# Optimization experiments

Measured on AMD Instinct MI355X. Metric: run time of the kernel, lower is better.

## Reference

```python
import jax, jax.numpy as jnp
import numpy as np

TEMPERATURE = 0.07


def setup_inputs() -> dict:
    key = jax.random.key(0)
    k1, k2, k3 = jax.random.split(key, 3)
    b, num_proposals, num_phrases, f = 128, 100, 16, 512
    img_features = jax.random.normal(k1, (b, num_proposals, f), dtype=jnp.float32)
    text_features = jax.random.normal(k2, (b, num_phrases, f), dtype=jnp.float32)
    labels = jax.random.randint(k3, (b, b), 0, 2, dtype=jnp.int64)
    return {"img_features": img_features, "text_features": text_features, "labels": labels}


def reference(img_features, text_features, labels):
    # att_matrix[b,d,t,i] = <text[b,t,:], img[d,i,:]>
    att_matrix = jnp.einsum('btf,dif->bdti', text_features, img_features)
    argmax_box = att_matrix.max(axis=3)        # [b, d, t]  max over proposals
    score_matrix = argmax_box.mean(axis=2)     # [b, d]     mean over phrases
    score_exp = jnp.exp(score_matrix / TEMPERATURE)
    return score_exp
```

## Files before the change

kernel.cpp:

```cpp
#include <hip/hip_runtime.h>
#include <hip/hip_bf16.h>
#include <stdint.h>


typedef __attribute__((ext_vector_type(4))) int    v4i;
typedef __attribute__((ext_vector_type(8))) int    v8i;
typedef __attribute__((ext_vector_type(4))) float  f32x4;

constexpr int Bb = 128;
constexpr int P  = 100;
constexpr int T  = 16;
constexpr int F  = 512;
constexpr float TEMP = 0.07f;

constexpr int BM   = 128;
constexpr int NCG  = 7;
constexpr int GSZ  = 16 * 16 * 32;
constexpr int NXCD = 8;

__global__ __launch_bounds__(256)
void cvt2_kernel(const float* __restrict__ img, const float* __restrict__ txt,
                 uint8_t* __restrict__ imgb, uint8_t* __restrict__ txtb) {
  __shared__ __align__(16) uint8_t lds[16 * 528];
  const int g  = blockIdx.x;
  const int t  = threadIdx.x;
  const int lr = t >> 4;
  const int c  = t & 15;

  const float* src;
  uint8_t* dst;
  if (g < Bb * NCG) {
    const int d  = g / NCG;
    const int cg = g - d * NCG;
    const int row  = cg * 16 + lr;
    const int prow = row < P ? row : (P - 1);
    src = img + ((size_t)d * P + prow) * F + c * 32;
    dst = imgb + (size_t)g * GSZ;
  } else {
    const int rg = g - Bb * NCG;
    src = txt + ((size_t)rg * 16 + lr) * F + c * 32;
    dst = txtb + (size_t)rg * GSZ;
  }

  int wd[8];
  #pragma unroll
  for (int j = 0; j < 4; j++) {
    float4 v0 = *(const float4*)(src + j * 8);
    float4 v1 = *(const float4*)(src + j * 8 + 4);
    int lo = __builtin_amdgcn_cvt_pk_fp8_f32(v0.x, v0.y, 0, false);
    lo     = __builtin_amdgcn_cvt_pk_fp8_f32(v0.z, v0.w, lo, true);
    int hi = __builtin_amdgcn_cvt_pk_fp8_f32(v1.x, v1.y, 0, false);
    hi     = __builtin_amdgcn_cvt_pk_fp8_f32(v1.z, v1.w, hi, true);
    wd[j * 2] = lo; wd[j * 2 + 1] = hi;
  }
  uint8_t* lp = &lds[lr * 528 + c * 32];
  *(v4i*)lp        = v4i{wd[0], wd[1], wd[2], wd[3]};
  *(v4i*)(lp + 16) = v4i{wd[4], wd[5], wd[6], wd[7]};
  __syncthreads();

  const uint8_t* rp = &lds[(t & 15) * 528 + (t >> 4) * 32];
  v4i lo = *(const v4i*)rp;
  v4i hi = *(const v4i*)(rp + 16);
  *(v4i*)(dst + t * 32)      = lo;
  *(v4i*)(dst + t * 32 + 16) = hi;
}

template<bool FUSED>
__global__ __launch_bounds__(256)
void score_kernel(const void* __restrict__ imgp, const void* __restrict__ txtp,
                  float* __restrict__ out) {
  __shared__ float red[BM][2];

  const int L    = blockIdx.x;
  const int xcd  = L & (NXCD - 1);
  const int slot = L >> 3;
  const int d    = xcd * 16 + (slot >> 4);
  const int b0   = (slot & 15) * (BM / T);

  const int tid  = threadIdx.x;
  const int lane = tid & 63;
  const int w    = tid >> 6;
  const int q    = lane >> 4;
  const int n    = lane & 15;
  const int mh   = w & 1;
  const int nh   = w >> 1;
  const int NCT  = 4 - nh;

  f32x4 acc[4][4] = {};

  if constexpr (!FUSED) {
    const uint8_t* gt = (const uint8_t*)txtp;
    const uint8_t* gi = (const uint8_t*)imgp;
    int agrp[4], bgrp[4];
    #pragma unroll
    for (int rt = 0; rt < 4; rt++) agrp[rt] = b0 + mh * 4 + rt;
    #pragma unroll
    for (int ct = 0; ct < 4; ct++) bgrp[ct] = d * NCG + nh * 4 + ct;

    #pragma unroll
    for (int k4 = 0; k4 < 4; k4++) {
      const int kc  = k4 * 4 + q;
      const int off = kc * 512 + n * 32;
      v8i a[4];
      #pragma unroll
      for (int rt = 0; rt < 4; rt++) {
        const uint8_t* p = gt + (size_t)agrp[rt] * GSZ + off;
        v4i lo = *(const v4i*)p;
        v4i hi = *(const v4i*)(p + 16);
        a[rt] = __builtin_shufflevector(lo, hi, 0, 1, 2, 3, 4, 5, 6, 7);
      }
      #pragma unroll
      for (int ct = 0; ct < 4; ct++) {
        if (ct < NCT) {
          const uint8_t* p = gi + (size_t)bgrp[ct] * GSZ + off;
          v4i lo = *(const v4i*)p;
          v4i hi = *(const v4i*)(p + 16);
          v8i b = __builtin_shufflevector(lo, hi, 0, 1, 2, 3, 4, 5, 6, 7);
          __builtin_amdgcn_s_setprio(1);
          #pragma unroll
          for (int rt = 0; rt < 4; rt++)
            acc[rt][ct] = __builtin_amdgcn_mfma_scale_f32_16x16x128_f8f6f4(
                a[rt], b, acc[rt][ct], 0, 0, 0, 127, 0, 127);
          __builtin_amdgcn_s_setprio(0);
        }
      }
    }
  } else {
    auto frag32 = [](const float* p) -> v8i {
      int wd[8];
      #pragma unroll
      for (int j = 0; j < 4; j++) {
        float4 v0 = *(const float4*)(p + j * 8);
        float4 v1 = *(const float4*)(p + j * 8 + 4);
        int lo = __builtin_amdgcn_cvt_pk_fp8_f32(v0.x, v0.y, 0, false);
        lo     = __builtin_amdgcn_cvt_pk_fp8_f32(v0.z, v0.w, lo, true);
        int hi = __builtin_amdgcn_cvt_pk_fp8_f32(v1.x, v1.y, 0, false);
        hi     = __builtin_amdgcn_cvt_pk_fp8_f32(v1.z, v1.w, hi, true);
        wd[j * 2] = lo; wd[j * 2 + 1] = hi;
      }
      return v8i{wd[0], wd[1], wd[2], wd[3], wd[4], wd[5], wd[6], wd[7]};
    };
    const float* gt = (const float*)txtp;
    const float* gi = (const float*)imgp;
    int arow[4], brow[4];
    #pragma unroll
    for (int rt = 0; rt < 4; rt++) arow[rt] = b0 * T + mh * 64 + rt * 16 + n;
    #pragma unroll
    for (int ct = 0; ct < 4; ct++) {
      const int col = nh * 64 + ct * 16 + n;
      brow[ct] = d * P + (col < P ? col : 0);
    }
    #pragma unroll
    for (int k4 = 0; k4 < 4; k4++) {
      const int koff = k4 * 128 + q * 32;
      v8i a[4];
      #pragma unroll
      for (int rt = 0; rt < 4; rt++)
        a[rt] = frag32(gt + (size_t)arow[rt] * F + koff);
      #pragma unroll
      for (int ct = 0; ct < 4; ct++) {
        if (ct < NCT) {
          v8i b = frag32(gi + (size_t)brow[ct] * F + koff);
          #pragma unroll
          for (int rt = 0; rt < 4; rt++)
            acc[rt][ct] = __builtin_amdgcn_mfma_scale_f32_16x16x128_f8f6f4(
                a[rt], b, acc[rt][ct], 0, 0, 0, 127, 0, 127);
        }
      }
    }
  }

  #pragma unroll
  for (int rt = 0; rt < 4; rt++) {
    float m[4];
    #pragma unroll
    for (int r = 0; r < 4; r++) {
      float v = -3.0e38f;
      #pragma unroll
      for (int ct = 0; ct < 4; ct++) {
        const bool valid = (ct < NCT) && (nh * 64 + ct * 16 + n) < P;
        const float x = acc[rt][ct][r];
        v = valid ? fmaxf(v, x) : v;
      }
      #pragma unroll
      for (int off = 1; off < 16; off <<= 1)
        v = fmaxf(v, __shfl_xor(v, off));
      m[r] = v;
    }
    if (n == 0) {
      #pragma unroll
      for (int r = 0; r < 4; r++)
        red[mh * 64 + rt * 16 + q * 4 + r][nh] = m[r];
    }
  }
  __syncthreads();

  if (tid < BM / T) {
    float s = 0.f;
    #pragma unroll
    for (int t = 0; t < T; t++) {
      const int r = tid * T + t;
      s += fmaxf(red[r][0], red[r][1]);
    }
    const float arg = fminf(s * (1.0f / (T * TEMP)), 88.0f);
    out[(size_t)(b0 + tid) * Bb + d] = expf(arg);
  }
}

extern "C" void kernel_launch(void* const* d_in, const int* in_sizes, int n_in,
                              void* d_out, int out_size, void* d_ws, size_t ws_size,
                              hipStream_t stream) {
  const float* img = (const float*)d_in[0];
  const float* txt = (const float*)d_in[1];
  float* out = (float*)d_out;

  const size_t imgN = (size_t)Bb * NCG * GSZ;
  const size_t txtN = (size_t)Bb * GSZ;
  const size_t need = imgN + txtN;

  dim3 grid((Bb * Bb * T) / BM);
  if (ws_size >= need) {
    uint8_t* imgb = (uint8_t*)d_ws;
    uint8_t* txtb = imgb + imgN;
    cvt2_kernel<<<Bb * NCG + Bb, 256, 0, stream>>>(img, txt, imgb, txtb);
    score_kernel<false><<<grid, 256, 0, stream>>>(imgb, txtb, out);
  } else {
    score_kernel<true><<<grid, 256, 0, stream>>>(img, txt, out);
  }
}
```

Baseline: 108.9 us.

## Stage image fp8 tiles in LDS via direct global-to-LDS loads with A double-buffering

The conversion kernel now writes fp8 fragments in a layout where each lane's 16-byte halves sit 1024 bytes apart, so loads are fully coalesced. The score kernel copies the whole per-d image tile (7 groups) into LDS with global_load_lds, then reads B fragments from LDS and double-buffers A fragments from global across k-steps. The aim is to cut redundant global/L2 traffic for B and overlap loads with MFMA. The cost is about 57KB of LDS per block, which lowers occupancy, and the setprio hints are dropped.

After: 102.4 us. 1.06x faster.

```diff
diff --git a/kernel.cpp b/kernel.cpp
--- a/kernel.cpp
+++ b/kernel.cpp
@@ -58,17 +58,23 @@
   *(v4i*)(lp + 16) = v4i{wd[4], wd[5], wd[6], wd[7]};
   __syncthreads();
 
-  const uint8_t* rp = &lds[(t & 15) * 528 + (t >> 4) * 32];
+  const int n  = t & 15;
+  const int kc = t >> 4;
+  const int k4 = kc >> 2;
+  const int q  = kc & 3;
+  const uint8_t* rp = &lds[n * 528 + kc * 32];
   v4i lo = *(const v4i*)rp;
   v4i hi = *(const v4i*)(rp + 16);
-  *(v4i*)(dst + t * 32)      = lo;
-  *(v4i*)(dst + t * 32 + 16) = hi;
+  uint8_t* op = dst + k4 * 2048 + q * 256 + n * 16;
+  *(v4i*)op          = lo;
+  *(v4i*)(op + 1024) = hi;
 }
 
 template<bool FUSED>
 __global__ __launch_bounds__(256)
 void score_kernel(const void* __restrict__ imgp, const void* __restrict__ txtp,
                   float* __restrict__ out) {
+  __shared__ __align__(16) uint8_t Bs[FUSED ? 16 : NCG * GSZ];
   __shared__ float red[BM][2];
 
   const int L    = blockIdx.x;
@@ -91,40 +97,66 @@
   if constexpr (!FUSED) {
     const uint8_t* gt = (const uint8_t*)txtp;
     const uint8_t* gi = (const uint8_t*)imgp;
-    int agrp[4], bgrp[4];
-    #pragma unroll
-    for (int rt = 0; rt < 4; rt++) agrp[rt] = b0 + mh * 4 + rt;
-    #pragma unroll
-    for (int ct = 0; ct < 4; ct++) bgrp[ct] = d * NCG + nh * 4 + ct;
-
-    #pragma unroll
-    for (int k4 = 0; k4 < 4; k4++) {
-      const int kc  = k4 * 4 + q;
-      const int off = kc * 512 + n * 32;
-      v8i a[4];
+
+    {
+      const uint8_t* base = gi + (size_t)d * NCG * GSZ;
+      #pragma unroll
+      for (int i = 0; i < 14; i++) {
+        const int c = i * 4 + w;
+        const uint8_t* ga = base + (size_t)c * 1024 + lane * 16;
+        __builtin_amdgcn_global_load_lds(
+            (const __attribute__((address_space(1))) void*)ga,
+            (__attribute__((address_space(3))) void*)&Bs[c * 1024], 16, 0, 0);
+      }
+    }
+
+    const uint8_t* abase = gt + (size_t)(b0 + mh * 4) * GSZ;
+    const int off = lane * 16;
+
+    auto ldA = [&](v8i (&a)[4], int k4) {
       #pragma unroll
       for (int rt = 0; rt < 4; rt++) {
-        const uint8_t* p = gt + (size_t)agrp[rt] * GSZ + off;
+        const uint8_t* p = abase + (size_t)rt * GSZ + k4 * 2048 + off;
         v4i lo = *(const v4i*)p;
-        v4i hi = *(const v4i*)(p + 16);
+        v4i hi = *(const v4i*)(p + 1024);
         a[rt] = __builtin_shufflevector(lo, hi, 0, 1, 2, 3, 4, 5, 6, 7);
       }
-      #pragma unroll
-      for (int ct = 0; ct < 4; ct++) {
+    };
+    auto ldB = [&](v8i (&b)[4], int k4) {
+      #pragma unroll
+      for (int ct = 0; ct < 4; ct++)
         if (ct < NCT) {
-          const uint8_t* p = gi + (size_t)bgrp[ct] * GSZ + off;
+          const uint8_t* p = &Bs[(nh * 4 + ct) * GSZ + k4 * 2048 + off];
           v4i lo = *(const v4i*)p;
-          v4i hi = *(const v4i*)(p + 16);
-          v8i b = __builtin_shufflevector(lo, hi, 0, 1, 2, 3, 4, 5, 6, 7);
-          __builtin_amdgcn_s_setprio(1);
+          v4i hi = *(const v4i*)(p + 1024);
+          b[ct] = __builtin_shufflevector(lo, hi, 0, 1, 2, 3, 4, 5, 6, 7);
+        }
+    };
+    auto mfmaset = [&](v8i (&a)[4], v8i (&b)[4]) {
+      #pragma unroll
+      for (int ct = 0; ct < 4; ct++)
+        if (ct < NCT)
           #pragma unroll
           for (int rt = 0; rt < 4; rt++)
             acc[rt][ct] = __builtin_amdgcn_mfma_scale_f32_16x16x128_f8f6f4(
-                a[rt], b, acc[rt][ct], 0, 0, 0, 127, 0, 127);
-          __builtin_amdgcn_s_setprio(0);
-        }
-      }
-    }
+                a[rt], b[ct], acc[rt][ct], 0, 0, 0, 127, 0, 127);
+    };
+
+    v8i aA[4], aB[4], bb[4];
+    ldA(aA, 0);
+    ldA(aB, 1);
+    __syncthreads();
+
+    ldB(bb, 0);
+    mfmaset(aA, bb);
+    ldA(aA, 2);
+    ldB(bb, 1);
+    mfmaset(aB, bb);
+    ldA(aB, 3);
+    ldB(bb, 2);
+    mfmaset(aA, bb);
+    ldB(bb, 3);
+    mfmaset(aB, bb);
   } else {
     auto frag32 = [](const float* p) -> v8i {
       int wd[8];
@@ -168,6 +200,7 @@
         }
       }
     }
+    __syncthreads();
   }
 
   #pragma unroll
```
